# Kernel tuning notes

Hardware: AMD Instinct MI355X
Metric: run time of the kernel (lower is better)

The kernel has to match this reference:

```python
import jax, jax.numpy as jnp
import numpy as np

EMBED_DIM = 1152
NUM_HEADS = 16
HEAD_DIM = EMBED_DIM // NUM_HEADS  # 72
TOTAL_TOKENS = 4096


def setup_inputs() -> dict:
    key = jax.random.key(0)
    k_x, k_wqkv, k_bqkv, k_wout, k_bout = jax.random.split(key, 5)
    hidden_states = jax.random.normal(k_x, (1, TOTAL_TOKENS, EMBED_DIM), dtype=jnp.float32)
    # fused QKV projection (use_qkv_parallel=True): weight [3*E, E], bias [3*E]
    w_qkv = jax.random.normal(k_wqkv, (3 * EMBED_DIM, EMBED_DIM), dtype=jnp.float32) * 0.02
    b_qkv = jax.random.normal(k_bqkv, (3 * EMBED_DIM,), dtype=jnp.float32) * 0.02
    # output projection [E, E]
    w_out = jax.random.normal(k_wout, (EMBED_DIM, EMBED_DIM), dtype=jnp.float32) * 0.02
    b_out = jax.random.normal(k_bout, (EMBED_DIM,), dtype=jnp.float32) * 0.02
    # 8 ragged sequences packed to 4096 tokens total
    cu_seqlens = jnp.array([0, 300, 900, 1500, 2124, 2600, 3100, 3624, 4096], dtype=jnp.int32)
    return {
        "hidden_states": hidden_states,
        "w_qkv": w_qkv,
        "b_qkv": b_qkv,
        "w_out": w_out,
        "b_out": b_out,
        "cu_seqlens": cu_seqlens,
        "max_seqlen": 1024,
    }


def _varlen_attention(x, w_qkv, b_qkv, w_out, b_out, cu_seqlens):
    # x: [T, E] packed tokens
    T = x.shape[0]
    qkv = x @ w_qkv.T + b_qkv                         # [T, 3E]
    q, k, v = jnp.split(qkv, 3, axis=-1)
    q = q.reshape(T, NUM_HEADS, HEAD_DIM)
    k = k.reshape(T, NUM_HEADS, HEAD_DIM)
    v = v.reshape(T, NUM_HEADS, HEAD_DIM)
    scale = HEAD_DIM ** -0.5
    # block-diagonal (per-sequence) attention via segment-id mask
    seg = jnp.searchsorted(cu_seqlens[1:], jnp.arange(T, dtype=jnp.int32), side="right")
    same_seq = seg[:, None] == seg[None, :]           # [T, T] bool
    scores = jnp.einsum("thd,shd->hts", q, k) * scale  # [H, T, T]
    scores = jnp.where(same_seq[None, :, :], scores, jnp.float32(-1e30))
    attn = jax.nn.softmax(scores, axis=-1)
    out = jnp.einsum("hts,shd->thd", attn, v).reshape(T, EMBED_DIM)
    return out @ w_out.T + b_out                      # [T, E]


def reference(hidden_states, w_qkv, b_qkv, w_out, b_out, cu_seqlens, max_seqlen):
    # max_seqlen is unused by the module (VisionAttention computes internally)
    out = _varlen_attention(hidden_states[0], w_qkv, b_qkv, w_out, b_out, cu_seqlens)
    return out[None]  # (1, total_tokens, embed_dim)
```

## Files before the change

kernel.cpp:

```cpp
#include <hip/hip_runtime.h>
#include <hip/hip_bf16.h>
#include <stdint.h>

typedef __hip_bfloat16 bf16;
typedef __attribute__((ext_vector_type(8))) short short8;
typedef __attribute__((ext_vector_type(4))) float float4v;

#define MFMA16(a, b, c) __builtin_amdgcn_mfma_f32_16x16x32_bf16((a), (b), (c), 0, 0, 0)

static __device__ __forceinline__ short f2bf(float f) {
    bf16 h = __float2bfloat16(f);
    return *reinterpret_cast<short*>(&h);
}

static __device__ __forceinline__ void gl2lds16(const void* g, void* l) {
    __builtin_amdgcn_global_load_lds(
        (const __attribute__((address_space(1))) void*)g,
        (__attribute__((address_space(3))) void*)l, 16, 0, 0);
}

__global__ __launch_bounds__(256) void cvt_all(
    const float* __restrict__ a, bf16* __restrict__ A, int na,
    const float* __restrict__ b, bf16* __restrict__ B, int nb,
    const float* __restrict__ c, bf16* __restrict__ C, int nc)
{
    int i = (blockIdx.x * 256 + threadIdx.x) * 8;
    const float* src; bf16* dst;
    if (i < na)                 { src = a; dst = A; }
    else if (i < na + nb)       { i -= na; src = b; dst = B; }
    else                        { i -= na + nb; src = c; dst = C; if (i >= nc) return; }
    const float4v x0 = *(const float4v*)(src + i);
    const float4v x1 = *(const float4v*)(src + i + 4);
    short8 v;
#pragma unroll
    for (int q = 0; q < 4; ++q) { v[q] = f2bf(x0[q]); v[q + 4] = f2bf(x1[q]); }
    *(short8*)(dst + i) = v;
}

__global__ __launch_bounds__(256) void gemm_qkv(
    const bf16* __restrict__ X, const bf16* __restrict__ W,
    const float* __restrict__ bias,
    bf16* __restrict__ Qh, bf16* __restrict__ Kh, bf16* __restrict__ Vt,
    int M, int K)
{
    __shared__ __align__(16) bf16 SMEM[16384];
    bf16* As = SMEM;
    bf16* Bs = SMEM + 8192;

    const int tid  = threadIdx.x;
    const int wave = tid >> 6;
    const int lane = tid & 63;
    const int quad = lane >> 4;
    const int l16  = lane & 15;
    const int m0 = blockIdx.x * 128;
    const int n0 = blockIdx.y * 128;
    const int wm = (wave >> 1) * 64;
    const int wn = (wave & 1) * 64;

    const int lrow   = lane >> 2;
    const int lchunk = lane & 3;

    const int nIt = K >> 5;

    float4v acc[4][4];
    const float4v zf = {0.f, 0.f, 0.f, 0.f};
#pragma unroll
    for (int i = 0; i < 4; ++i)
#pragma unroll
        for (int j = 0; j < 4; ++j) acc[i][j] = zf;

    auto stage = [&](int buf, int k0) {
#pragma unroll
        for (int ii = 0; ii < 2; ++ii) {
            const int rbase = wave * 32 + ii * 16;
            const int r  = rbase + lrow;
            const int sc = lchunk ^ ((r >> 1) & 3);
            gl2lds16(&X[(size_t)(m0 + r) * K + k0 + sc * 8], &As[buf * 4096 + rbase * 32]);
            gl2lds16(&W[(size_t)(n0 + r) * K + k0 + sc * 8], &Bs[buf * 4096 + rbase * 32]);
        }
    };

    stage(0, 0);

    for (int it = 0; it < nIt; ++it) {
        __syncthreads();
        if (it + 1 < nIt) stage((it + 1) & 1, (it + 1) * 32);

        const int b = it & 1;
        short8 af[4], bfr[4];
#pragma unroll
        for (int i = 0; i < 4; ++i) {
            const int r = wm + i * 16 + l16;
            af[i] = *(const short8*)&As[b * 4096 + r * 32 + (quad ^ ((r >> 1) & 3)) * 8];
        }
#pragma unroll
        for (int j = 0; j < 4; ++j) {
            const int r = wn + j * 16 + l16;
            bfr[j] = *(const short8*)&Bs[b * 4096 + r * 32 + (quad ^ ((r >> 1) & 3)) * 8];
        }
#pragma unroll
        for (int i = 0; i < 4; ++i)
#pragma unroll
            for (int j = 0; j < 4; ++j)
                acc[i][j] = MFMA16(af[i], bfr[j], acc[i][j]);
    }

    bf16* T = SMEM;

    if (n0 >= 2304) {
#pragma unroll 1
        for (int half = 0; half < 2; ++half) {
            __syncthreads();
            if ((wave & 1) == half) {
#pragma unroll
                for (int j = 0; j < 4; ++j) {
                    const int col = n0 + wn + j * 16 + l16;
                    const float bb = bias[col];
#pragma unroll
                    for (int i = 0; i < 4; ++i)
#pragma unroll
                        for (int r = 0; r < 4; ++r)
                            T[(j * 16 + l16) * 136 + wm + i * 16 + quad * 4 + r] =
                                __float2bfloat16(acc[i][j][r] + bb);
                }
            }
            __syncthreads();
            const int dd   = tid >> 2;
            const int tok0 = (tid & 3) * 32;
            const int colg = n0 + half * 64 + dd - 2304;
            const int hh   = colg / 72;
            const int dm   = colg - hh * 72;
            bf16* dst = &Vt[((size_t)hh * 72 + dm) * 4096 + m0 + tok0];
#pragma unroll
            for (int k = 0; k < 4; ++k)
                *(short8*)(dst + k * 8) = *(const short8*)&T[dd * 136 + tok0 + k * 8];
        }
        return;
    }

#pragma unroll 1
    for (int half = 0; half < 2; ++half) {
        __syncthreads();
        if ((wave >> 1) == half) {
#pragma unroll
            for (int j = 0; j < 4; ++j) {
                const int col = n0 + wn + j * 16 + l16;
                const float bb = bias[col];
#pragma unroll
                for (int i = 0; i < 4; ++i)
#pragma unroll
                    for (int r = 0; r < 4; ++r)
                        T[(i * 16 + quad * 4 + r) * 136 + wn + j * 16 + l16] =
                            __float2bfloat16(acc[i][j][r] + bb);
            }
        }
        __syncthreads();
        const int rloc = tid >> 2;
        const int row  = m0 + half * 64 + rloc;
        const int c0   = (tid & 3) * 32;
#pragma unroll
        for (int k = 0; k < 4; ++k) {
            const int colg = n0 + c0 + k * 8;
            const bool isQ = (colg < 1152);
            const int cc = isQ ? colg : colg - 1152;
            const int hh = cc / 72;
            const int dd = cc - hh * 72;
            bf16* dst = (isQ ? Qh : Kh) + ((size_t)hh * 4096 + row) * 72 + dd;
            *(short8*)dst = *(const short8*)&T[rloc * 136 + c0 + k * 8];
        }
    }
}

__global__ __launch_bounds__(256) void gemm_out(
    const bf16* __restrict__ X, const bf16* __restrict__ W,
    const float* __restrict__ bias, float* __restrict__ Cout,
    int M, int N, int K)
{
    __shared__ __align__(16) bf16 As[2][128 * 32];
    __shared__ __align__(16) bf16 Bs[2][64 * 32];

    const int tid  = threadIdx.x;
    const int wave = tid >> 6;
    const int lane = tid & 63;
    const int quad = lane >> 4;
    const int l16  = lane & 15;
    const int m0 = blockIdx.x * 128;
    const int n0 = blockIdx.y * 64;
    const int wm = (wave >> 1) * 64;
    const int wn = (wave & 1) * 32;

    const int lrow   = lane >> 2;
    const int lchunk = lane & 3;

    const int nIt = K >> 5;

    float4v acc[4][2];
    const float4v zf = {0.f, 0.f, 0.f, 0.f};
#pragma unroll
    for (int i = 0; i < 4; ++i)
#pragma unroll
        for (int j = 0; j < 2; ++j) acc[i][j] = zf;

    auto stage = [&](int buf, int k0) {
#pragma unroll
        for (int ii = 0; ii < 2; ++ii) {
            const int rbase = wave * 32 + ii * 16;
            const int r  = rbase + lrow;
            const int sc = lchunk ^ ((r >> 1) & 3);
            gl2lds16(&X[(size_t)(m0 + r) * K + k0 + sc * 8], &As[buf][rbase * 32]);
        }
        {
            const int rbase = wave * 16;
            const int r  = rbase + lrow;
            const int sc = lchunk ^ ((r >> 1) & 3);
            gl2lds16(&W[(size_t)(n0 + r) * K + k0 + sc * 8], &Bs[buf][rbase * 32]);
        }
    };

    stage(0, 0);

    for (int it = 0; it < nIt; ++it) {
        __syncthreads();
        if (it + 1 < nIt) stage((it + 1) & 1, (it + 1) * 32);

        const int b = it & 1;
        short8 af[4], bfr[2];
#pragma unroll
        for (int i = 0; i < 4; ++i) {
            const int r = wm + i * 16 + l16;
            af[i] = *(const short8*)&As[b][r * 32 + (quad ^ ((r >> 1) & 3)) * 8];
        }
#pragma unroll
        for (int j = 0; j < 2; ++j) {
            const int r = wn + j * 16 + l16;
            bfr[j] = *(const short8*)&Bs[b][r * 32 + (quad ^ ((r >> 1) & 3)) * 8];
        }
#pragma unroll
        for (int i = 0; i < 4; ++i)
#pragma unroll
            for (int j = 0; j < 2; ++j)
                acc[i][j] = MFMA16(af[i], bfr[j], acc[i][j]);
    }

#pragma unroll
    for (int j = 0; j < 2; ++j) {
        const int col = n0 + wn + j * 16 + l16;
        const float bb = bias[col];
#pragma unroll
        for (int i = 0; i < 4; ++i) {
#pragma unroll
            for (int r = 0; r < 4; ++r) {
                const int row = m0 + wm + i * 16 + quad * 4 + r;
                Cout[(size_t)row * N + col] = acc[i][j][r] + bb;
            }
        }
    }
}

__global__ __launch_bounds__(256) void attn_varlen(
    const bf16* __restrict__ Qh, const bf16* __restrict__ Kh,
    const bf16* __restrict__ Vt,
    const int* __restrict__ cu, bf16* __restrict__ AO)
{
    const float scale = 0.11785113019775793f;
    __shared__ __align__(16) bf16 Ks[2][64 * 72];
    __shared__ __align__(16) bf16 Vs[2][80 * 64];
    __shared__ __align__(16) bf16 Ps[4][16 * 72];

    const int tid  = threadIdx.x;
    const int wave = tid >> 6;
    const int lane = tid & 63;
    const int quad = lane >> 4;
    const int l16  = lane & 15;
    const int h  = blockIdx.x & 15;
    const int qb = blockIdx.x >> 4;

    int seq_end = 0, q0 = -1, accb = 0, seq_start = 0;
    for (int i = 0; i < 8; ++i) {
        const int st = cu[i], en = cu[i + 1];
        const int nb = (en - st + 63) >> 6;
        if (q0 < 0 && qb < accb + nb) {
            seq_start = st; seq_end = en; q0 = st + (qb - accb) * 64;
        }
        accb += nb;
    }
    if (q0 < 0) return;

    const bf16 onev  = __float2bfloat16(1.0f);
    const bf16 zerov = __float2bfloat16(0.0f);
    for (int t = tid; t < 1024; t += 256) {
        const int b = t >> 9, rr = (t >> 6) & 7, cc = t & 63;
        Vs[b][(72 + rr) * 64 + cc] = (rr == 0) ? onev : zerov;
    }

    const short8 z8 = {0, 0, 0, 0, 0, 0, 0, 0};

    int qrow_f = q0 + wave * 16 + l16; if (qrow_f > 4095) qrow_f = 4095;
    const bf16* qp = &Qh[((size_t)h * 4096 + qrow_f) * 72];
    short8 aq[3];
    aq[0] = *(const short8*)(qp + quad * 8);
    aq[1] = *(const short8*)(qp + 32 + quad * 8);
    aq[2] = (quad == 0) ? *(const short8*)(qp + 64) : z8;

    const bf16* kbase = &Kh[(size_t)h * 4096 * 72];
    auto stage = [&](int buf, int kv0) {
        const bf16* ksrc = kbase + (size_t)kv0 * 72;
        for (int i = wave; i < 9; i += 4)
            gl2lds16(ksrc + i * 512 + lane * 8, &Ks[buf][i * 512]);
        for (int i = wave; i < 9; i += 4) {
            const int d  = i * 8 + (lane >> 3);
            const int ch = (lane & 7) ^ (d & 7);
            gl2lds16(&Vt[((size_t)h * 72 + d) * 4096 + kv0 + ch * 8],
                     &Vs[buf][i * 512]);
        }
    };

    const float4v zf = {0.f, 0.f, 0.f, 0.f};
    float4v oacc[5];
#pragma unroll
    for (int d = 0; d < 5; ++d) oacc[d] = zf;

    const int kvbeg = seq_start & ~63;
    stage(0, kvbeg);

    for (int kv0 = kvbeg; kv0 < seq_end; kv0 += 64) {
        const int b = ((kv0 - kvbeg) >> 6) & 1;
        __syncthreads();
        if (kv0 + 64 < seq_end) stage(b ^ 1, kv0 + 64);

        float4v sc[4];
#pragma unroll
        for (int nt = 0; nt < 4; ++nt) {
            const bf16* kb = &Ks[b][(nt * 16 + l16) * 72];
            float4v s = zf;
            s = MFMA16(aq[0], *(const short8*)(kb + quad * 8), s);
            s = MFMA16(aq[1], *(const short8*)(kb + 32 + quad * 8), s);
            s = MFMA16(aq[2], (quad == 0) ? *(const short8*)(kb + 64) : z8, s);
            sc[nt] = s;
        }

#pragma unroll
        for (int nt = 0; nt < 4; ++nt) {
            const int kv = kv0 + nt * 16 + l16;
            const bool ok = (kv >= seq_start) && (kv < seq_end);
#pragma unroll
            for (int r = 0; r < 4; ++r) {
                const float p = ok ? __expf(sc[nt][r] * scale) : 0.f;
                Ps[wave][(quad * 4 + r) * 72 + nt * 16 + l16] = __float2bfloat16(p);
            }
        }

        const short8 ap0 = *(const short8*)&Ps[wave][l16 * 72 + quad * 8];
        const short8 ap1 = *(const short8*)&Ps[wave][l16 * 72 + 32 + quad * 8];

#pragma unroll
        for (int dt = 0; dt < 5; ++dt) {
            const int vr = dt * 16 + l16;
            const bf16* vb = &Vs[b][vr * 64];
            const short8 bv0 = *(const short8*)(vb + ((quad ^ (vr & 7)) * 8));
            const short8 bv1 = *(const short8*)(vb + (((quad + 4) ^ (vr & 7)) * 8));
            oacc[dt] = MFMA16(ap0, bv0, oacc[dt]);
            oacc[dt] = MFMA16(ap1, bv1, oacc[dt]);
        }
    }

#pragma unroll
    for (int r = 0; r < 4; ++r) {
        const int qrow = q0 + wave * 16 + quad * 4 + r;
        const float lv = __shfl(oacc[4][r], (lane & 48) | 8);
        if (qrow < seq_end) {
            const float inv = (lv > 0.f) ? (1.0f / lv) : 0.f;
#pragma unroll
            for (int d = 0; d < 5; ++d) {
                const int dim = d * 16 + l16;
                if (dim < 72)
                    AO[(size_t)qrow * 1152 + h * 72 + dim] =
                        __float2bfloat16(oacc[d][r] * inv);
            }
        }
    }
}

extern "C" void kernel_launch(void* const* d_in, const int* in_sizes, int n_in,
                              void* d_out, int out_size, void* d_ws, size_t ws_size,
                              hipStream_t stream)
{
    const float* Xf   = (const float*)d_in[0];
    const float* Wqkv = (const float*)d_in[1];
    const float* Bqkv = (const float*)d_in[2];
    const float* Wout = (const float*)d_in[3];
    const float* Bout = (const float*)d_in[4];
    const int*   cu   = (const int*)d_in[5];

    const size_t X16_B  = (size_t)4096 * 1152 * 2;
    const size_t WQ16_B = (size_t)3456 * 1152 * 2;
    const size_t WO16_B = (size_t)1152 * 1152 * 2;
    const size_t H_B    = (size_t)16 * 4096 * 72 * 2;

    char* ws = (char*)d_ws;
    bf16* X16  = (bf16*)ws;
    bf16* WQ16 = (bf16*)(ws + X16_B);
    bf16* WO16 = (bf16*)(ws + X16_B + WQ16_B);
    bf16* Qh   = (bf16*)(ws + X16_B + WQ16_B + WO16_B);
    bf16* Kh   = (bf16*)(ws + X16_B + WQ16_B + WO16_B + H_B);
    bf16* Vt   = (bf16*)(ws + X16_B + WQ16_B + WO16_B + 2 * H_B);
    bf16* AO   = (bf16*)(ws + X16_B + WQ16_B + WO16_B + 3 * H_B);
    float* Out = (float*)d_out;

    dim3 blk(256);
    cvt_all<<<dim3(4896), blk, 0, stream>>>(Xf, X16, 4096 * 1152,
                                            Wqkv, WQ16, 3456 * 1152,
                                            Wout, WO16, 1152 * 1152);

    gemm_qkv<<<dim3(32, 27), blk, 0, stream>>>(X16, WQ16, Bqkv,
                                               Qh, Kh, Vt, 4096, 1152);
    attn_varlen<<<dim3(72 * 16), blk, 0, stream>>>(Qh, Kh, Vt, cu, AO);
    gemm_out<<<dim3(32, 18), blk, 0, stream>>>(AO, WO16, Bout, Out,
                                               4096, 1152, 1152);
}
```

Measured before the change: 202.3 us.

## Rewrite QKV GEMM as 256x256 tile, 8-wave ping-pong pipelined kernel

```diff
diff --git a/kernel.cpp b/kernel.cpp
--- a/kernel.cpp
+++ b/kernel.cpp
@@ -21,14 +21,27 @@
 
 __global__ __launch_bounds__(256) void cvt_all(
     const float* __restrict__ a, bf16* __restrict__ A, int na,
-    const float* __restrict__ b, bf16* __restrict__ B, int nb,
+    const float* __restrict__ b, bf16* __restrict__ B, int nbd, int nbt,
     const float* __restrict__ c, bf16* __restrict__ C, int nc)
 {
     int i = (blockIdx.x * 256 + threadIdx.x) * 8;
     const float* src; bf16* dst;
-    if (i < na)                 { src = a; dst = A; }
-    else if (i < na + nb)       { i -= na; src = b; dst = B; }
-    else                        { i -= na + nb; src = c; dst = C; if (i >= nc) return; }
+    if (i < na) { src = a; dst = A; }
+    else {
+        i -= na;
+        if (i < nbt) {
+            if (i >= nbd) {
+                const short8 z = {0, 0, 0, 0, 0, 0, 0, 0};
+                *(short8*)(B + i) = z;
+                return;
+            }
+            src = b; dst = B;
+        } else {
+            i -= nbt;
+            if (i >= nc) return;
+            src = c; dst = C;
+        }
+    }
     const float4v x0 = *(const float4v*)(src + i);
     const float4v x1 = *(const float4v*)(src + i + 4);
     short8 v;
@@ -37,136 +50,174 @@
     *(short8*)(dst + i) = v;
 }
 
-__global__ __launch_bounds__(256) void gemm_qkv(
+static __device__ __forceinline__ void phase_sync() {
+    __builtin_amdgcn_s_barrier();
+    asm volatile("s_waitcnt lgkmcnt(0)" ::: "memory");
+    __builtin_amdgcn_sched_barrier(0);
+    __builtin_amdgcn_s_setprio(1);
+}
+static __device__ __forceinline__ void phase_end() {
+    __builtin_amdgcn_s_setprio(0);
+    __builtin_amdgcn_s_barrier();
+}
+
+__global__ __launch_bounds__(512) void gemm_qkv(
     const bf16* __restrict__ X, const bf16* __restrict__ W,
     const float* __restrict__ bias,
-    bf16* __restrict__ Qh, bf16* __restrict__ Kh, bf16* __restrict__ Vt,
-    int M, int K)
+    bf16* __restrict__ Qh, bf16* __restrict__ Kh, bf16* __restrict__ Vt)
 {
-    __shared__ __align__(16) bf16 SMEM[16384];
-    bf16* As = SMEM;
-    bf16* Bs = SMEM + 8192;
+    __shared__ __align__(16) bf16 SM[65536];
 
     const int tid  = threadIdx.x;
     const int wave = tid >> 6;
     const int lane = tid & 63;
     const int quad = lane >> 4;
     const int l16  = lane & 15;
-    const int m0 = blockIdx.x * 128;
-    const int n0 = blockIdx.y * 128;
-    const int wm = (wave >> 1) * 64;
-    const int wn = (wave & 1) * 64;
-
-    const int lrow   = lane >> 2;
-    const int lchunk = lane & 3;
-
-    const int nIt = K >> 5;
-
-    float4v acc[4][4];
+    const int wr   = wave >> 2;
+    const int wc   = wave & 3;
+    const int m0 = blockIdx.x * 256;
+    const int n0 = blockIdx.y * 256;
+    const int cch = (lane & 7) ^ (lane >> 3);
+    const int KT = 18;
+
+    float4v acc[8][4];
     const float4v zf = {0.f, 0.f, 0.f, 0.f};
 #pragma unroll
-    for (int i = 0; i < 4; ++i)
+    for (int i = 0; i < 8; ++i)
 #pragma unroll
         for (int j = 0; j < 4; ++j) acc[i][j] = zf;
 
-    auto stage = [&](int buf, int k0) {
-#pragma unroll
-        for (int ii = 0; ii < 2; ++ii) {
-            const int rbase = wave * 32 + ii * 16;
-            const int r  = rbase + lrow;
-            const int sc = lchunk ^ ((r >> 1) & 3);
-            gl2lds16(&X[(size_t)(m0 + r) * K + k0 + sc * 8], &As[buf * 4096 + rbase * 32]);
-            gl2lds16(&W[(size_t)(n0 + r) * K + k0 + sc * 8], &Bs[buf * 4096 + rbase * 32]);
-        }
-    };
-
-    stage(0, 0);
-
-    for (int it = 0; it < nIt; ++it) {
-        __syncthreads();
-        if (it + 1 < nIt) stage((it + 1) & 1, (it + 1) * 32);
-
-        const int b = it & 1;
-        short8 af[4], bfr[4];
-#pragma unroll
-        for (int i = 0; i < 4; ++i) {
-            const int r = wm + i * 16 + l16;
-            af[i] = *(const short8*)&As[b * 4096 + r * 32 + (quad ^ ((r >> 1) & 3)) * 8];
-        }
-#pragma unroll
-        for (int j = 0; j < 4; ++j) {
-            const int r = wn + j * 16 + l16;
-            bfr[j] = *(const short8*)&Bs[b * 4096 + r * 32 + (quad ^ ((r >> 1) & 3)) * 8];
-        }
-#pragma unroll
-        for (int i = 0; i < 4; ++i)
-#pragma unroll
-            for (int j = 0; j < 4; ++j)
-                acc[i][j] = MFMA16(af[i], bfr[j], acc[i][j]);
-    }
-
-    bf16* T = SMEM;
-
-    if (n0 >= 2304) {
+    auto stageA = [&](int buf, int kt, int h) {
+#pragma unroll
+        for (int i = 0; i < 2; ++i) {
+            const int ls = (wave * 2 + i) * 8 + (lane >> 3);
+            const int grow = m0 + ((ls >> 6) << 7) + (h << 6) + (ls & 63);
+            gl2lds16(&X[(size_t)grow * 1152 + kt * 64 + cch * 8],
+                     &SM[buf * 16384 + (h * 128 + (wave * 2 + i) * 8) * 64]);
+        }
+    };
+    auto stageB = [&](int buf, int kt, int h) {
+#pragma unroll
+        for (int i = 0; i < 2; ++i) {
+            const int ls = (wave * 2 + i) * 8 + (lane >> 3);
+            const int grow = n0 + ((ls >> 5) << 6) + (h << 5) + (ls & 31);
+            gl2lds16(&W[(size_t)grow * 1152 + kt * 64 + cch * 8],
+                     &SM[32768 + buf * 16384 + (h * 128 + (wave * 2 + i) * 8) * 64]);
+        }
+    };
+
+    auto ldA = [&](int buf, int mh, short8* a) {
+#pragma unroll
+        for (int fm = 0; fm < 4; ++fm)
+#pragma unroll
+            for (int ks = 0; ks < 2; ++ks) {
+                const int sr = mh * 128 + wr * 64 + fm * 16 + l16;
+                const int pos = (ks * 4 + quad) ^ (l16 & 7);
+                a[fm * 2 + ks] = *(const short8*)&SM[buf * 16384 + sr * 64 + pos * 8];
+            }
+    };
+    auto ldB = [&](int buf, int nh, short8* bv) {
+#pragma unroll
+        for (int fn = 0; fn < 2; ++fn)
+#pragma unroll
+            for (int ks = 0; ks < 2; ++ks) {
+                const int sr = nh * 128 + wc * 32 + fn * 16 + l16;
+                const int pos = (ks * 4 + quad) ^ (l16 & 7);
+                bv[fn * 2 + ks] = *(const short8*)&SM[32768 + buf * 16384 + sr * 64 + pos * 8];
+            }
+    };
+    auto mfma_q = [&](int mh, int nh, const short8* a, const short8* bv) {
+#pragma unroll
+        for (int fm = 0; fm < 4; ++fm)
+#pragma unroll
+            for (int fn = 0; fn < 2; ++fn)
+#pragma unroll
+                for (int ks = 0; ks < 2; ++ks)
+                    acc[mh * 4 + fm][nh * 2 + fn] =
+                        MFMA16(a[fm * 2 + ks], bv[fn * 2 + ks], acc[mh * 4 + fm][nh * 2 + fn]);
+    };
+
+    stageA(0, 0, 0); stageB(0, 0, 1);
+    stageA(0, 0, 1); stageB(0, 0, 0);
+    stageA(1, 1, 0); stageB(1, 1, 1);
+    asm volatile("s_waitcnt vmcnt(4)" ::: "memory");
+    __builtin_amdgcn_s_barrier();
+
 #pragma unroll 1
-        for (int half = 0; half < 2; ++half) {
-            __syncthreads();
-            if ((wave & 1) == half) {
-#pragma unroll
-                for (int j = 0; j < 4; ++j) {
-                    const int col = n0 + wn + j * 16 + l16;
-                    const float bb = bias[col];
-#pragma unroll
-                    for (int i = 0; i < 4; ++i)
+    for (int t = 0; t < KT; ++t) {
+        const int cbuf = t & 1, obuf = cbuf ^ 1;
+        short8 a[8], bv[4];
+        ldA(cbuf, 0, a);
+        ldB(cbuf, 0, bv);
+        if (t + 1 < KT) stageA(obuf, t + 1, 1);
+        phase_sync(); mfma_q(0, 0, a, bv); phase_end();
+        ldB(cbuf, 1, bv);
+        if (t + 1 < KT) stageB(obuf, t + 1, 0);
+        phase_sync(); mfma_q(0, 1, a, bv); phase_end();
+        ldA(cbuf, 1, a);
+        if (t + 2 < KT) stageA(cbuf, t + 2, 0);
+        phase_sync(); mfma_q(1, 1, a, bv); phase_end();
+        ldB(cbuf, 0, bv);
+        if (t + 2 < KT) stageB(cbuf, t + 2, 1);
+        if (t + 2 < KT)      { asm volatile("s_waitcnt vmcnt(4)" ::: "memory"); }
+        else if (t + 1 < KT) { asm volatile("s_waitcnt vmcnt(0)" ::: "memory"); }
+        phase_sync(); mfma_q(1, 0, a, bv); phase_end();
+    }
+
+    __syncthreads();
+    const int colbase = n0 + wc * 64;
+    if (colbase < 3456) {
+        bf16* T = &SM[wave * 8192];
+        const bool isV = (colbase >= 2304);
+        float bcol[4];
+#pragma unroll
+        for (int cj = 0; cj < 4; ++cj) bcol[cj] = bias[colbase + cj * 16 + l16];
+
+#pragma unroll 1
+        for (int mh = 0; mh < 2; ++mh) {
+            if (!isV) {
+#pragma unroll
+                for (int cj = 0; cj < 4; ++cj)
+#pragma unroll
+                    for (int fm = 0; fm < 4; ++fm)
 #pragma unroll
                         for (int r = 0; r < 4; ++r)
-                            T[(j * 16 + l16) * 136 + wm + i * 16 + quad * 4 + r] =
-                                __float2bfloat16(acc[i][j][r] + bb);
+                            T[(fm * 16 + quad * 4 + r) * 72 + cj * 16 + l16] =
+                                __float2bfloat16(acc[mh * 4 + fm][cj][r] + bcol[cj]);
+            } else {
+#pragma unroll
+                for (int cj = 0; cj < 4; ++cj)
+#pragma unroll
+                    for (int fm = 0; fm < 4; ++fm)
+#pragma unroll
+                        for (int r = 0; r < 4; ++r)
+                            T[(cj * 16 + l16) * 72 + fm * 16 + quad * 4 + r] =
+                                __float2bfloat16(acc[mh * 4 + fm][cj][r] + bcol[cj]);
+            }
+            asm volatile("s_waitcnt lgkmcnt(0)" ::: "memory");
+            const int rg0 = m0 + wr * 128 + mh * 64;
+            if (!isV) {
+                const bool isQ = colbase < 1152;
+                const int cb2 = isQ ? colbase : colbase - 1152;
+                bf16* outp = isQ ? Qh : Kh;
+#pragma unroll
+                for (int ch = 0; ch < 8; ++ch) {
+                    const int colg = cb2 + ch * 8;
+                    const int hh = colg / 72;
+                    const int dd = colg - hh * 72;
+                    *(short8*)(outp + ((size_t)hh * 4096 + rg0 + lane) * 72 + dd) =
+                        *(const short8*)&T[lane * 72 + ch * 8];
                 }
-            }
-            __syncthreads();
-            const int dd   = tid >> 2;
-            const int tok0 = (tid & 3) * 32;
-            const int colg = n0 + half * 64 + dd - 2304;
-            const int hh   = colg / 72;
-            const int dm   = colg - hh * 72;
-            bf16* dst = &Vt[((size_t)hh * 72 + dm) * 4096 + m0 + tok0];
-#pragma unroll
-            for (int k = 0; k < 4; ++k)
-                *(short8*)(dst + k * 8) = *(const short8*)&T[dd * 136 + tok0 + k * 8];
-        }
-        return;
-    }
-
-#pragma unroll 1
-    for (int half = 0; half < 2; ++half) {
-        __syncthreads();
-        if ((wave >> 1) == half) {
-#pragma unroll
-            for (int j = 0; j < 4; ++j) {
-                const int col = n0 + wn + j * 16 + l16;
-                const float bb = bias[col];
-#pragma unroll
-                for (int i = 0; i < 4; ++i)
-#pragma unroll
-                    for (int r = 0; r < 4; ++r)
-                        T[(i * 16 + quad * 4 + r) * 136 + wn + j * 16 + l16] =
-                            __float2bfloat16(acc[i][j][r] + bb);
-            }
-        }
-        __syncthreads();
-        const int rloc = tid >> 2;
-        const int row  = m0 + half * 64 + rloc;
-        const int c0   = (tid & 3) * 32;
-#pragma unroll
-        for (int k = 0; k < 4; ++k) {
-            const int colg = n0 + c0 + k * 8;
-            const bool isQ = (colg < 1152);
-            const int cc = isQ ? colg : colg - 1152;
-            const int hh = cc / 72;
-            const int dd = cc - hh * 72;
-            bf16* dst = (isQ ? Qh : Kh) + ((size_t)hh * 4096 + row) * 72 + dd;
-            *(short8*)dst = *(const short8*)&T[rloc * 136 + c0 + k * 8];
+            } else {
+                const int cd = colbase - 2304 + lane;
+                const int hh = cd / 72;
+                const int dm = cd - hh * 72;
+                bf16* dst = &Vt[((size_t)hh * 72 + dm) * 4096 + rg0];
+#pragma unroll
+                for (int ch = 0; ch < 8; ++ch)
+                    *(short8*)(dst + ch * 8) = *(const short8*)&T[lane * 72 + ch * 8];
+            }
+            asm volatile("s_waitcnt lgkmcnt(0)" ::: "memory");
         }
     }
 }
@@ -393,7 +444,7 @@
     const int*   cu   = (const int*)d_in[5];
 
     const size_t X16_B  = (size_t)4096 * 1152 * 2;
-    const size_t WQ16_B = (size_t)3456 * 1152 * 2;
+    const size_t WQ16_B = (size_t)3584 * 1152 * 2;
     const size_t WO16_B = (size_t)1152 * 1152 * 2;
     const size_t H_B    = (size_t)16 * 4096 * 72 * 2;
 
@@ -408,12 +459,11 @@
     float* Out = (float*)d_out;
 
     dim3 blk(256);
-    cvt_all<<<dim3(4896), blk, 0, stream>>>(Xf, X16, 4096 * 1152,
-                                            Wqkv, WQ16, 3456 * 1152,
+    cvt_all<<<dim3(4968), blk, 0, stream>>>(Xf, X16, 4096 * 1152,
+                                            Wqkv, WQ16, 3456 * 1152, 3584 * 1152,
                                             Wout, WO16, 1152 * 1152);
 
-    gemm_qkv<<<dim3(32, 27), blk, 0, stream>>>(X16, WQ16, Bqkv,
-                                               Qh, Kh, Vt, 4096, 1152);
+    gemm_qkv<<<dim3(16, 14), dim3(512), 0, stream>>>(X16, WQ16, Bqkv, Qh, Kh, Vt);
     attn_varlen<<<dim3(72 * 16), blk, 0, stream>>>(Qh, Kh, Vt, cu, AO);
     gemm_out<<<dim3(32, 18), blk, 0, stream>>>(AO, WO16, Bout, Out,
                                                4096, 1152, 1152);
```

New measurement: 219.0 us. +8.3%, slower.

## Load K and V tiles directly from global memory instead of LDS double buffering

Applied to the files above, without the earlier changes.

```diff
diff --git a/kernel.cpp b/kernel.cpp
--- a/kernel.cpp
+++ b/kernel.cpp
@@ -263,8 +263,6 @@
     const int* __restrict__ cu, bf16* __restrict__ AO)
 {
     const float scale = 0.11785113019775793f;
-    __shared__ __align__(16) bf16 Ks[2][64 * 72];
-    __shared__ __align__(16) bf16 Vs[2][80 * 64];
     __shared__ __align__(16) bf16 Ps[4][16 * 72];
 
     const int tid  = threadIdx.x;
@@ -286,14 +284,9 @@
     }
     if (q0 < 0) return;
 
-    const bf16 onev  = __float2bfloat16(1.0f);
-    const bf16 zerov = __float2bfloat16(0.0f);
-    for (int t = tid; t < 1024; t += 256) {
-        const int b = t >> 9, rr = (t >> 6) & 7, cc = t & 63;
-        Vs[b][(72 + rr) * 64 + cc] = (rr == 0) ? onev : zerov;
-    }
-
     const short8 z8 = {0, 0, 0, 0, 0, 0, 0, 0};
+    const short   o1 = f2bf(1.0f);
+    const short8 one8 = {o1, o1, o1, o1, o1, o1, o1, o1};
 
     int qrow_f = q0 + wave * 16 + l16; if (qrow_f > 4095) qrow_f = 4095;
     const bf16* qp = &Qh[((size_t)h * 4096 + qrow_f) * 72];
@@ -303,35 +296,18 @@
     aq[2] = (quad == 0) ? *(const short8*)(qp + 64) : z8;
 
     const bf16* kbase = &Kh[(size_t)h * 4096 * 72];
-    auto stage = [&](int buf, int kv0) {
-        const bf16* ksrc = kbase + (size_t)kv0 * 72;
-        for (int i = wave; i < 9; i += 4)
-            gl2lds16(ksrc + i * 512 + lane * 8, &Ks[buf][i * 512]);
-        for (int i = wave; i < 9; i += 4) {
-            const int d  = i * 8 + (lane >> 3);
-            const int ch = (lane & 7) ^ (d & 7);
-            gl2lds16(&Vt[((size_t)h * 72 + d) * 4096 + kv0 + ch * 8],
-                     &Vs[buf][i * 512]);
-        }
-    };
+    const bf16* vbase = &Vt[(size_t)h * 72 * 4096];
 
     const float4v zf = {0.f, 0.f, 0.f, 0.f};
     float4v oacc[5];
 #pragma unroll
     for (int d = 0; d < 5; ++d) oacc[d] = zf;
 
-    const int kvbeg = seq_start & ~63;
-    stage(0, kvbeg);
-
-    for (int kv0 = kvbeg; kv0 < seq_end; kv0 += 64) {
-        const int b = ((kv0 - kvbeg) >> 6) & 1;
-        __syncthreads();
-        if (kv0 + 64 < seq_end) stage(b ^ 1, kv0 + 64);
-
+    for (int kv0 = seq_start & ~63; kv0 < seq_end; kv0 += 64) {
         float4v sc[4];
 #pragma unroll
         for (int nt = 0; nt < 4; ++nt) {
-            const bf16* kb = &Ks[b][(nt * 16 + l16) * 72];
+            const bf16* kb = kbase + (size_t)(kv0 + nt * 16 + l16) * 72;
             float4v s = zf;
             s = MFMA16(aq[0], *(const short8*)(kb + quad * 8), s);
             s = MFMA16(aq[1], *(const short8*)(kb + 32 + quad * 8), s);
@@ -356,9 +332,20 @@
 #pragma unroll
         for (int dt = 0; dt < 5; ++dt) {
             const int vr = dt * 16 + l16;
-            const bf16* vb = &Vs[b][vr * 64];
-            const short8 bv0 = *(const short8*)(vb + ((quad ^ (vr & 7)) * 8));
-            const short8 bv1 = *(const short8*)(vb + (((quad + 4) ^ (vr & 7)) * 8));
+            short8 bv0, bv1;
+            if (dt < 4) {
+                const bf16* vb = vbase + (size_t)vr * 4096 + kv0;
+                bv0 = *(const short8*)(vb + quad * 8);
+                bv1 = *(const short8*)(vb + 32 + quad * 8);
+            } else if (l16 < 8) {
+                const bf16* vb = vbase + (size_t)vr * 4096 + kv0;
+                bv0 = *(const short8*)(vb + quad * 8);
+                bv1 = *(const short8*)(vb + 32 + quad * 8);
+            } else if (l16 == 8) {
+                bv0 = one8; bv1 = one8;
+            } else {
+                bv0 = z8;   bv1 = z8;
+            }
             oacc[dt] = MFMA16(ap0, bv0, oacc[dt]);
             oacc[dt] = MFMA16(ap1, bv1, oacc[dt]);
         }
```

After: 230.6 us. +14.0%, slower.

## Load V fragments directly from global into registers, drop V LDS staging

Applied to the files above, without the earlier changes.

```diff
diff --git a/kernel.cpp b/kernel.cpp
--- a/kernel.cpp
+++ b/kernel.cpp
@@ -264,8 +264,7 @@
 {
     const float scale = 0.11785113019775793f;
     __shared__ __align__(16) bf16 Ks[2][64 * 72];
-    __shared__ __align__(16) bf16 Vs[2][80 * 64];
-    __shared__ __align__(16) bf16 Ps[4][16 * 72];
+    __shared__ __align__(16) bf16 Ps[4][16 * 76];
 
     const int tid  = threadIdx.x;
     const int wave = tid >> 6;
@@ -286,14 +285,9 @@
     }
     if (q0 < 0) return;
 
-    const bf16 onev  = __float2bfloat16(1.0f);
-    const bf16 zerov = __float2bfloat16(0.0f);
-    for (int t = tid; t < 1024; t += 256) {
-        const int b = t >> 9, rr = (t >> 6) & 7, cc = t & 63;
-        Vs[b][(72 + rr) * 64 + cc] = (rr == 0) ? onev : zerov;
-    }
-
     const short8 z8 = {0, 0, 0, 0, 0, 0, 0, 0};
+    const short   o1 = f2bf(1.0f);
+    const short8 one8 = {o1, o1, o1, o1, o1, o1, o1, o1};
 
     int qrow_f = q0 + wave * 16 + l16; if (qrow_f > 4095) qrow_f = 4095;
     const bf16* qp = &Qh[((size_t)h * 4096 + qrow_f) * 72];
@@ -303,16 +297,12 @@
     aq[2] = (quad == 0) ? *(const short8*)(qp + 64) : z8;
 
     const bf16* kbase = &Kh[(size_t)h * 4096 * 72];
-    auto stage = [&](int buf, int kv0) {
+    const bf16* vbase = &Vt[(size_t)h * 72 * 4096];
+
+    auto stageK = [&](int buf, int kv0) {
         const bf16* ksrc = kbase + (size_t)kv0 * 72;
         for (int i = wave; i < 9; i += 4)
             gl2lds16(ksrc + i * 512 + lane * 8, &Ks[buf][i * 512]);
-        for (int i = wave; i < 9; i += 4) {
-            const int d  = i * 8 + (lane >> 3);
-            const int ch = (lane & 7) ^ (d & 7);
-            gl2lds16(&Vt[((size_t)h * 72 + d) * 4096 + kv0 + ch * 8],
-                     &Vs[buf][i * 512]);
-        }
     };
 
     const float4v zf = {0.f, 0.f, 0.f, 0.f};
@@ -321,12 +311,25 @@
     for (int d = 0; d < 5; ++d) oacc[d] = zf;
 
     const int kvbeg = seq_start & ~63;
-    stage(0, kvbeg);
+    stageK(0, kvbeg);
 
     for (int kv0 = kvbeg; kv0 < seq_end; kv0 += 64) {
         const int b = ((kv0 - kvbeg) >> 6) & 1;
         __syncthreads();
-        if (kv0 + 64 < seq_end) stage(b ^ 1, kv0 + 64);
+
+        short8 bv0[5], bv1[5];
+#pragma unroll
+        for (int dt = 0; dt < 5; ++dt) {
+            const int vr = dt * 16 + l16;
+            if (dt < 4 || l16 < 8) {
+                const bf16* vb = vbase + (size_t)vr * 4096 + kv0;
+                bv0[dt] = *(const short8*)(vb + quad * 8);
+                bv1[dt] = *(const short8*)(vb + 32 + quad * 8);
+            } else if (l16 == 8) { bv0[dt] = one8; bv1[dt] = one8; }
+            else                 { bv0[dt] = z8;   bv1[dt] = z8; }
+        }
+
+        if (kv0 + 64 < seq_end) stageK(b ^ 1, kv0 + 64);
 
         float4v sc[4];
 #pragma unroll
@@ -346,21 +349,17 @@
 #pragma unroll
             for (int r = 0; r < 4; ++r) {
                 const float p = ok ? __expf(sc[nt][r] * scale) : 0.f;
-                Ps[wave][(quad * 4 + r) * 72 + nt * 16 + l16] = __float2bfloat16(p);
+                Ps[wave][(quad * 4 + r) * 76 + nt * 16 + l16] = __float2bfloat16(p);
             }
         }
 
-        const short8 ap0 = *(const short8*)&Ps[wave][l16 * 72 + quad * 8];
-        const short8 ap1 = *(const short8*)&Ps[wave][l16 * 72 + 32 + quad * 8];
+        const short8 ap0 = *(const short8*)&Ps[wave][l16 * 76 + quad * 8];
+        const short8 ap1 = *(const short8*)&Ps[wave][l16 * 76 + 32 + quad * 8];
 
 #pragma unroll
         for (int dt = 0; dt < 5; ++dt) {
-            const int vr = dt * 16 + l16;
-            const bf16* vb = &Vs[b][vr * 64];
-            const short8 bv0 = *(const short8*)(vb + ((quad ^ (vr & 7)) * 8));
-            const short8 bv1 = *(const short8*)(vb + (((quad + 4) ^ (vr & 7)) * 8));
-            oacc[dt] = MFMA16(ap0, bv0, oacc[dt]);
-            oacc[dt] = MFMA16(ap1, bv1, oacc[dt]);
+            oacc[dt] = MFMA16(ap0, bv0[dt], oacc[dt]);
+            oacc[dt] = MFMA16(ap1, bv1[dt], oacc[dt]);
         }
     }
 
```

Result: slower. 232.8 us (+15.1%).
